# Kernel optimization log

Measured on AMD Instinct MI355X. Metric: run time of the kernel, lower is better.

The kernel has to match this reference:

```python
import jax, jax.numpy as jnp
import numpy as np

N = 100000
E = 3200000
HOP = 10

def setup_inputs() -> dict:
    key = jax.random.key(0)
    ks = jax.random.split(key, 10)
    n_in, n_hid, n_out = 512, 256, 64
    x = jax.random.normal(ks[0], (N, n_in), dtype=jnp.float32)
    edge_row = jax.random.randint(ks[1], (E,), 0, N, dtype=jnp.int32)
    edge_col = jax.random.randint(ks[2], (E,), 0, N, dtype=jnp.int32)
    # row-normalized-ish positive edge values (like a transition matrix)
    edge_vals = jax.random.uniform(ks[3], (E,), dtype=jnp.float32) / 32.0
    A2 = jax.random.uniform(ks[4], (N, 1), dtype=jnp.float32)
    # xavier-ish init scaled down for numerical sanity
    W1 = jax.random.normal(ks[5], (n_in, n_hid), dtype=jnp.float32) * (2.0 / (n_in + n_hid)) ** 0.5
    b1 = jnp.zeros((n_hid,), dtype=jnp.float32)
    W3 = jax.random.normal(ks[6], (n_hid, n_hid), dtype=jnp.float32) * (2.0 / (2 * n_hid)) ** 0.5
    b3 = jnp.zeros((n_hid,), dtype=jnp.float32)
    W2 = jax.random.normal(ks[7], (n_hid, n_out), dtype=jnp.float32) * (2.0 / (n_hid + n_out)) ** 0.5
    b2 = jnp.zeros((n_out,), dtype=jnp.float32)
    return {"x": x, "edge_row": edge_row, "edge_col": edge_col, "edge_vals": edge_vals,
            "A2": A2, "W1": W1, "b1": b1, "W3": W3, "b3": b3, "W2": W2, "b2": b2}

def _spmm(edge_row, edge_col, edge_vals, h):
    # sparse [N,N] @ dense [N,F] via gather + segment_sum
    msgs = edge_vals[:, None] * h[edge_col]          # [E, F]
    return jax.ops.segment_sum(msgs, edge_row, num_segments=N)

def reference(x, edge_row, edge_col, edge_vals, A2, W1, b1, W3, b3, W2, b2):
    # dropout layers are identity at eval time
    x0 = jax.nn.relu(x @ W1 + b1)                    # [N, n_hid]
    h = x0
    for _ in range(HOP):
        h = _spmm(edge_row, edge_col, edge_vals, h) + A2 * x0
        h = jax.nn.relu(h + h @ W3 + b3)
    return h @ W2 + b2                               # [N, n_out]
```

## Files before the change

kernel.cpp:

```cpp
#include <hip/hip_runtime.h>
#include <stdint.h>


typedef unsigned short bf16_t;
typedef __attribute__((ext_vector_type(8))) short bf16x8;
typedef __attribute__((ext_vector_type(4))) float f32x4;

__device__ __forceinline__ float bf2f(bf16_t u) {
    union { unsigned int i; float f; } v; v.i = ((unsigned int)u) << 16; return v.f;
}
__device__ __forceinline__ bf16_t f2bf(float f) {
    union { float f; unsigned int i; } v; v.f = f;
    unsigned int x = v.i;
    unsigned int r = (x + 0x7fffu + ((x >> 16) & 1u)) >> 16;
    return (bf16_t)r;
}

__global__ void zero_i32(int* __restrict__ p, int n) {
    int i = blockIdx.x * blockDim.x + threadIdx.x;
    if (i < n) p[i] = 0;
}

__global__ void transpose_w(const float* __restrict__ W, bf16_t* __restrict__ Wt,
                            int K, int N) {
    int i = blockIdx.x * blockDim.x + threadIdx.x;
    if (i < K * N) {
        int k = i / N, n = i % N;
        Wt[(size_t)n * K + k] = f2bf(W[i]);
    }
}

__global__ void count_edges(const int* __restrict__ er, int* __restrict__ cnt,
                            int E, int N) {
    int i = blockIdx.x * blockDim.x + threadIdx.x;
    if (i < E) {
        unsigned r = (unsigned)er[i];
        if (r < (unsigned)N) atomicAdd(&cnt[r], 1);
    }
}

__global__ __launch_bounds__(1024)
void scan_rows(int* cnt_cursor, int* __restrict__ row_ptr, int n) {
    __shared__ int sums[1024];
    int t = threadIdx.x;
    int chunk = (n + 1023) >> 10;
    int start = t * chunk;
    int end = min(start + chunk, n);
    int s = 0;
    for (int i = start; i < end; ++i) s += cnt_cursor[i];
    sums[t] = s;
    __syncthreads();
    for (int off = 1; off < 1024; off <<= 1) {
        int v = (t >= off) ? sums[t - off] : 0;
        __syncthreads();
        sums[t] += v;
        __syncthreads();
    }
    int run = (t == 0) ? 0 : sums[t - 1];
    for (int i = start; i < end; ++i) {
        int c = cnt_cursor[i];
        row_ptr[i] = run;
        run += c;
    }
    if (t == 1023) row_ptr[n] = sums[1023];
}

__global__ void init_bcur(const int* __restrict__ row_ptr, int* __restrict__ bcur,
                          int N, int NB) {
    int b = blockIdx.x * blockDim.x + threadIdx.x;
    if (b < NB) bcur[b] = row_ptr[min(b << 8, N)];
}

#define BIN_CHUNK 8192
#define NBMAX 392
__global__ __launch_bounds__(256)
void bin_edges(const int* __restrict__ er, const int* __restrict__ ec,
               const float* __restrict__ ev, int* __restrict__ bcur,
               int2* __restrict__ binned, int E, int N, int NB) {
    __shared__ int cnt[NBMAX];
    __shared__ int resv[NBMAX];
    int tid = threadIdx.x;
    int e0 = blockIdx.x * BIN_CHUNK;
    int n = min(BIN_CHUNK, E - e0);
    for (int b = tid; b < NB; b += 256) cnt[b] = 0;
    __syncthreads();
    for (int i = tid; i < n; i += 256) {
        unsigned r = (unsigned)er[e0 + i];
        if (r < (unsigned)N) atomicAdd(&cnt[r >> 8], 1);
    }
    __syncthreads();
    for (int b = tid; b < NB; b += 256) {
        int c = cnt[b];
        resv[b] = c ? atomicAdd(&bcur[b], c) : 0;
        cnt[b] = 0;
    }
    __syncthreads();
    for (int i = tid; i < n; i += 256) {
        unsigned r = (unsigned)er[e0 + i];
        if (r < (unsigned)N) {
            unsigned c = (unsigned)ec[e0 + i];
            float v = ev[e0 + i];
            if (c >= (unsigned)N) { c = 0; v = 0.f; }
            int b = (int)(r >> 8);
            int p = resv[b] + atomicAdd(&cnt[b], 1);
            binned[p] = make_int2((int)(((r & 255u) << 17) | c), __float_as_int(v));
        }
    }
}

#define BCAP 9216
__global__ __launch_bounds__(256)
void bucket_sort(const int* __restrict__ row_ptr, int2* __restrict__ csr, int N) {
    __shared__ int2 ent[BCAP];
    __shared__ int cnt[256];
    __shared__ int base[256];
    __shared__ int lcur[256];
    int b = blockIdx.x;
    int tid = threadIdx.x;
    int r0 = b << 8;
    int e0 = row_ptr[r0];
    int e1 = row_ptr[min(r0 + 256, N)];
    int n = e1 - e0;
    cnt[tid] = 0;
    __syncthreads();
    for (int i = tid; i < n; i += 256) {
        int2 p = csr[e0 + i];
        if (i < BCAP) ent[i] = p;
        atomicAdd(&cnt[((unsigned)p.x >> 17) & 255u], 1);
    }
    __syncthreads();
    int v0 = cnt[tid];
    for (int off = 1; off < 256; off <<= 1) {
        int u = (tid >= off) ? cnt[tid - off] : 0;
        __syncthreads();
        cnt[tid] += u;
        __syncthreads();
    }
    base[tid] = cnt[tid] - v0;
    lcur[tid] = 0;
    __syncthreads();
    for (int i = tid; i < n; i += 256) {
        int2 p = (i < BCAP) ? ent[i] : csr[e0 + i];
        int rl = (int)(((unsigned)p.x >> 17) & 255u);
        int d = base[rl] + atomicAdd(&lcur[rl], 1);
        csr[e0 + d] = make_int2(p.x & 0x1FFFF, p.y);
    }
}

__global__ __launch_bounds__(256)
void spmm_kernel(const int* __restrict__ row_ptr, const int2* __restrict__ csr,
                 const bf16_t* __restrict__ h, const bf16_t* __restrict__ x0,
                 const float* __restrict__ A2, bf16_t* __restrict__ s, int N) {
    int w = threadIdx.x >> 6;
    int lane = threadIdx.x & 63;
    int row = (blockIdx.x << 2) + w;
    if (row >= N) return;
    int fo = lane << 2;
    int base = (row << 8) + fo;
    float a2 = A2[row];
    ushort4 xv = *(const ushort4*)&x0[base];
    float acc0 = a2 * bf2f(xv.x);
    float acc1 = a2 * bf2f(xv.y);
    float acc2 = a2 * bf2f(xv.z);
    float acc3 = a2 * bf2f(xv.w);
    int e = row_ptr[row], e1 = row_ptr[row + 1];
    for (; e + 4 <= e1; e += 4) {
        int2 p0 = csr[e], p1 = csr[e + 1], p2 = csr[e + 2], p3 = csr[e + 3];
        ushort4 h0 = *(const ushort4*)&h[(p0.x << 8) + fo];
        ushort4 h1 = *(const ushort4*)&h[(p1.x << 8) + fo];
        ushort4 h2 = *(const ushort4*)&h[(p2.x << 8) + fo];
        ushort4 h3 = *(const ushort4*)&h[(p3.x << 8) + fo];
        float v0 = __int_as_float(p0.y), v1 = __int_as_float(p1.y);
        float v2 = __int_as_float(p2.y), v3 = __int_as_float(p3.y);
        acc0 += v0 * bf2f(h0.x); acc1 += v0 * bf2f(h0.y);
        acc2 += v0 * bf2f(h0.z); acc3 += v0 * bf2f(h0.w);
        acc0 += v1 * bf2f(h1.x); acc1 += v1 * bf2f(h1.y);
        acc2 += v1 * bf2f(h1.z); acc3 += v1 * bf2f(h1.w);
        acc0 += v2 * bf2f(h2.x); acc1 += v2 * bf2f(h2.y);
        acc2 += v2 * bf2f(h2.z); acc3 += v2 * bf2f(h2.w);
        acc0 += v3 * bf2f(h3.x); acc1 += v3 * bf2f(h3.y);
        acc2 += v3 * bf2f(h3.z); acc3 += v3 * bf2f(h3.w);
    }
    for (; e < e1; ++e) {
        int2 p = csr[e];
        ushort4 hv = *(const ushort4*)&h[(p.x << 8) + fo];
        float v = __int_as_float(p.y);
        acc0 += v * bf2f(hv.x); acc1 += v * bf2f(hv.y);
        acc2 += v * bf2f(hv.z); acc3 += v * bf2f(hv.w);
    }
    ushort4 o;
    o.x = f2bf(acc0); o.y = f2bf(acc1); o.z = f2bf(acc2); o.w = f2bf(acc3);
    *(ushort4*)&s[base] = o;
}

template <int WM, int WN, bool AF32, bool SKIP, bool RELU, typename CT>
__global__ __launch_bounds__(256)
void mfma_gemm(const void* __restrict__ Av, const bf16_t* __restrict__ Bt,
               const float* __restrict__ bias, CT* __restrict__ C,
               int M, int K, int Nfull) {
    constexpr int TM = WM * 64;
    constexpr int TN = WN * 64;
    __shared__ bf16_t As[TM * 32];
    __shared__ bf16_t Bs[TN * 32];
    const int tid = threadIdx.x;
    const int w = tid >> 6, lane = tid & 63;
    const int q = lane >> 4, l16 = lane & 15;
    const int bm = blockIdx.x * TM;
    const int bn = blockIdx.y * TN;
    const int wm = (w % WM) * 64;
    const int wn = (w / WM) * 64;

    f32x4 acc[4][4] = {};

    for (int k0 = 0; k0 < K; k0 += 32) {
        if constexpr (AF32) {
            const float* A = (const float*)Av;
            int row = tid >> 1;
            int gr = min(bm + row, M - 1);
            const float* src = A + (size_t)gr * K + k0 + (tid & 1) * 16;
            bf16_t* dst = As + row * 32 + (tid & 1) * 16;
            #pragma unroll
            for (int g = 0; g < 4; ++g) {
                float4 v = *(const float4*)(src + 4 * g);
                ushort4 u;
                u.x = f2bf(v.x); u.y = f2bf(v.y); u.z = f2bf(v.z); u.w = f2bf(v.w);
                *(ushort4*)(dst + 4 * g) = u;
            }
        } else {
            const bf16_t* A = (const bf16_t*)Av;
            #pragma unroll
            for (int r = 0; r < TM / 64; ++r) {
                int rowbase = r * 64 + w * 16;
                int row = rowbase + (lane >> 2);
                int gr = min(bm + row, M - 1);
                const bf16_t* gp = A + (size_t)gr * K + k0 + (lane & 3) * 8;
                bf16_t* lp = As + rowbase * 32 + lane * 8;
                __builtin_amdgcn_global_load_lds(
                    (const __attribute__((address_space(1))) unsigned int*)gp,
                    (__attribute__((address_space(3))) unsigned int*)lp, 16, 0, 0);
            }
        }
        #pragma unroll
        for (int r = 0; r < TN / 64; ++r) {
            int rowbase = r * 64 + w * 16;
            int row = rowbase + (lane >> 2);
            const bf16_t* gp = Bt + (size_t)(bn + row) * K + k0 + (lane & 3) * 8;
            bf16_t* lp = Bs + rowbase * 32 + lane * 8;
            __builtin_amdgcn_global_load_lds(
                (const __attribute__((address_space(1))) unsigned int*)gp,
                (__attribute__((address_space(3))) unsigned int*)lp, 16, 0, 0);
        }
        __syncthreads();

        bf16x8 afr[4], bfr[4];
        #pragma unroll
        for (int ms = 0; ms < 4; ++ms)
            afr[ms] = *(const bf16x8*)&As[(wm + ms * 16 + l16) * 32 + q * 8];
        #pragma unroll
        for (int ns = 0; ns < 4; ++ns)
            bfr[ns] = *(const bf16x8*)&Bs[(wn + ns * 16 + l16) * 32 + q * 8];
        #pragma unroll
        for (int ms = 0; ms < 4; ++ms)
            #pragma unroll
            for (int ns = 0; ns < 4; ++ns)
                acc[ms][ns] = __builtin_amdgcn_mfma_f32_16x16x32_bf16(
                    afr[ms], bfr[ns], acc[ms][ns], 0, 0, 0);
        __syncthreads();
    }

    const bf16_t* Askip = (const bf16_t*)Av;
    #pragma unroll
    for (int ms = 0; ms < 4; ++ms) {
        #pragma unroll
        for (int r = 0; r < 4; ++r) {
            int row = bm + wm + ms * 16 + q * 4 + r;
            if (row < M) {
                #pragma unroll
                for (int ns = 0; ns < 4; ++ns) {
                    int col = bn + wn + ns * 16 + l16;
                    float v = acc[ms][ns][r] + bias[col];
                    if constexpr (SKIP) v += bf2f(Askip[(size_t)row * K + col]);
                    if constexpr (RELU) v = fmaxf(v, 0.f);
                    if constexpr (sizeof(CT) == 2) C[(size_t)row * Nfull + col] = (CT)f2bf(v);
                    else                           C[(size_t)row * Nfull + col] = (CT)v;
                }
            }
        }
    }
}

extern "C" void kernel_launch(void* const* d_in, const int* in_sizes, int n_in,
                              void* d_out, int out_size, void* d_ws, size_t ws_size,
                              hipStream_t stream) {
    const float* x   = (const float*)d_in[0];
    const int* erow  = (const int*)d_in[1];
    const int* ecol  = (const int*)d_in[2];
    const float* ev  = (const float*)d_in[3];
    const float* A2  = (const float*)d_in[4];
    const float* W1  = (const float*)d_in[5];
    const float* b1  = (const float*)d_in[6];
    const float* W3  = (const float*)d_in[7];
    const float* b3  = (const float*)d_in[8];
    const float* W2  = (const float*)d_in[9];
    const float* b2  = (const float*)d_in[10];
    float* out = (float*)d_out;

    const int N   = in_sizes[4];
    const int E   = in_sizes[1];
    const int NIN = in_sizes[0] / N;
    const int NH  = in_sizes[6];
    const int NO  = in_sizes[10];
    if (NH != 256 || NIN != 512 || NO != 64) return;
    const int NB = (N + 255) >> 8;
    if (NB > NBMAX) return;

    char* ws = (char*)d_ws;
    size_t off = 0;
    auto alloc = [&](size_t bytes) -> void* {
        void* p = ws + off;
        off += (bytes + 255) & ~(size_t)255;
        return p;
    };
    bf16_t* x0     = (bf16_t*)alloc((size_t)N * NH * 2);
    bf16_t* hA     = (bf16_t*)alloc((size_t)N * NH * 2);
    bf16_t* hB     = (bf16_t*)alloc((size_t)N * NH * 2);
    int*   row_ptr = (int*)alloc((size_t)(N + 1) * 4);
    int*   counts  = (int*)alloc((size_t)N * 4);
    int*   bcur    = (int*)alloc((size_t)NB * 4);
    int2*  csr     = (int2*)alloc((size_t)E * 8);
    bf16_t* W1t    = (bf16_t*)alloc((size_t)NIN * NH * 2);
    bf16_t* W3t    = (bf16_t*)alloc((size_t)NH * NH * 2);
    bf16_t* W2t    = (bf16_t*)alloc((size_t)NH * NO * 2);
    if (off > ws_size) return;

    zero_i32<<<(N + 255) / 256, 256, 0, stream>>>(counts, N);
    count_edges<<<(E + 255) / 256, 256, 0, stream>>>(erow, counts, E, N);
    scan_rows<<<1, 1024, 0, stream>>>(counts, row_ptr, N);
    init_bcur<<<(NB + 255) / 256, 256, 0, stream>>>(row_ptr, bcur, N, NB);
    bin_edges<<<(E + BIN_CHUNK - 1) / BIN_CHUNK, 256, 0, stream>>>(
        erow, ecol, ev, bcur, csr, E, N, NB);
    bucket_sort<<<NB, 256, 0, stream>>>(row_ptr, csr, N);
    transpose_w<<<(NIN * NH + 255) / 256, 256, 0, stream>>>(W1, W1t, NIN, NH);
    transpose_w<<<(NH * NH + 255) / 256, 256, 0, stream>>>(W3, W3t, NH, NH);
    transpose_w<<<(NH * NO + 255) / 256, 256, 0, stream>>>(W2, W2t, NH, NO);

    dim3 g1((N + 127) / 128, NH / 128);
    mfma_gemm<2, 2, true, false, true, bf16_t><<<g1, 256, 0, stream>>>(
        x, W1t, b1, x0, N, NIN, NH);

    const bf16_t* hin = x0;
    for (int hop = 0; hop < 10; ++hop) {
        spmm_kernel<<<(N + 3) / 4, 256, 0, stream>>>(row_ptr, csr, hin, x0, A2, hB, N);
        mfma_gemm<2, 2, false, true, true, bf16_t><<<g1, 256, 0, stream>>>(
            hB, W3t, b3, hA, N, NH, NH);
        hin = hA;
    }

    dim3 g2((N + 255) / 256, 1);
    mfma_gemm<4, 1, false, false, false, float><<<g2, 256, 0, stream>>>(
        hA, W2t, b2, out, N, NH, NO);
}
```

Before: 3.439 ms.

## Split SpMM wavefront into two half-waves with 16-byte gathers and CSR prefetch

```diff
diff --git a/kernel.cpp b/kernel.cpp
--- a/kernel.cpp
+++ b/kernel.cpp
@@ -4,6 +4,7 @@
 
 typedef unsigned short bf16_t;
 typedef __attribute__((ext_vector_type(8))) short bf16x8;
+typedef __attribute__((ext_vector_type(8))) unsigned short u16x8;
 typedef __attribute__((ext_vector_type(4))) float f32x4;
 
 __device__ __forceinline__ float bf2f(bf16_t u) {
@@ -147,6 +148,12 @@
     }
 }
 
+__device__ __forceinline__ void fma8(float* acc, float v, u16x8 hv) {
+    #pragma unroll
+    for (int k = 0; k < 8; ++k)
+        acc[k] = fmaf(v, bf2f((bf16_t)hv[k]), acc[k]);
+}
+
 __global__ __launch_bounds__(256)
 void spmm_kernel(const int* __restrict__ row_ptr, const int2* __restrict__ csr,
                  const bf16_t* __restrict__ h, const bf16_t* __restrict__ x0,
@@ -155,42 +162,64 @@
     int lane = threadIdx.x & 63;
     int row = (blockIdx.x << 2) + w;
     if (row >= N) return;
-    int fo = lane << 2;
+    int half = lane >> 5;
+    int l32 = lane & 31;
+    int fo = l32 << 3;
     int base = (row << 8) + fo;
-    float a2 = A2[row];
-    ushort4 xv = *(const ushort4*)&x0[base];
-    float acc0 = a2 * bf2f(xv.x);
-    float acc1 = a2 * bf2f(xv.y);
-    float acc2 = a2 * bf2f(xv.z);
-    float acc3 = a2 * bf2f(xv.w);
+
+    float acc[8];
+    if (half == 0) {
+        float a2 = A2[row];
+        u16x8 xv = *(const u16x8*)&x0[base];
+        #pragma unroll
+        for (int k = 0; k < 8; ++k) acc[k] = a2 * bf2f((bf16_t)xv[k]);
+    } else {
+        #pragma unroll
+        for (int k = 0; k < 8; ++k) acc[k] = 0.f;
+    }
+
     int e = row_ptr[row], e1 = row_ptr[row + 1];
-    for (; e + 4 <= e1; e += 4) {
-        int2 p0 = csr[e], p1 = csr[e + 1], p2 = csr[e + 2], p3 = csr[e + 3];
-        ushort4 h0 = *(const ushort4*)&h[(p0.x << 8) + fo];
-        ushort4 h1 = *(const ushort4*)&h[(p1.x << 8) + fo];
-        ushort4 h2 = *(const ushort4*)&h[(p2.x << 8) + fo];
-        ushort4 h3 = *(const ushort4*)&h[(p3.x << 8) + fo];
-        float v0 = __int_as_float(p0.y), v1 = __int_as_float(p1.y);
-        float v2 = __int_as_float(p2.y), v3 = __int_as_float(p3.y);
-        acc0 += v0 * bf2f(h0.x); acc1 += v0 * bf2f(h0.y);
-        acc2 += v0 * bf2f(h0.z); acc3 += v0 * bf2f(h0.w);
-        acc0 += v1 * bf2f(h1.x); acc1 += v1 * bf2f(h1.y);
-        acc2 += v1 * bf2f(h1.z); acc3 += v1 * bf2f(h1.w);
-        acc0 += v2 * bf2f(h2.x); acc1 += v2 * bf2f(h2.y);
-        acc2 += v2 * bf2f(h2.z); acc3 += v2 * bf2f(h2.w);
-        acc0 += v3 * bf2f(h3.x); acc1 += v3 * bf2f(h3.y);
-        acc2 += v3 * bf2f(h3.z); acc3 += v3 * bf2f(h3.w);
-    }
-    for (; e < e1; ++e) {
+    int nb = (e1 - e) >> 3;
+    int2 q0, q1, q2, q3;
+    if (nb > 0) {
+        int eb = e + half;
+        q0 = csr[eb]; q1 = csr[eb + 2]; q2 = csr[eb + 4]; q3 = csr[eb + 6];
+    }
+    for (int b = 0; b < nb; ++b) {
+        int2 p0 = q0, p1 = q1, p2 = q2, p3 = q3;
+        if (b + 1 < nb) {
+            int eb = e + 8 + half;
+            q0 = csr[eb]; q1 = csr[eb + 2]; q2 = csr[eb + 4]; q3 = csr[eb + 6];
+        }
+        u16x8 h0 = *(const u16x8*)&h[(p0.x << 8) + fo];
+        u16x8 h1 = *(const u16x8*)&h[(p1.x << 8) + fo];
+        u16x8 h2 = *(const u16x8*)&h[(p2.x << 8) + fo];
+        u16x8 h3 = *(const u16x8*)&h[(p3.x << 8) + fo];
+        fma8(acc, __int_as_float(p0.y), h0);
+        fma8(acc, __int_as_float(p1.y), h1);
+        fma8(acc, __int_as_float(p2.y), h2);
+        fma8(acc, __int_as_float(p3.y), h3);
+        e += 8;
+    }
+    for (; e + 2 <= e1; e += 2) {
+        int2 p = csr[e + half];
+        u16x8 hv = *(const u16x8*)&h[(p.x << 8) + fo];
+        fma8(acc, __int_as_float(p.y), hv);
+    }
+    if (e < e1 && half == 0) {
         int2 p = csr[e];
-        ushort4 hv = *(const ushort4*)&h[(p.x << 8) + fo];
-        float v = __int_as_float(p.y);
-        acc0 += v * bf2f(hv.x); acc1 += v * bf2f(hv.y);
-        acc2 += v * bf2f(hv.z); acc3 += v * bf2f(hv.w);
-    }
-    ushort4 o;
-    o.x = f2bf(acc0); o.y = f2bf(acc1); o.z = f2bf(acc2); o.w = f2bf(acc3);
-    *(ushort4*)&s[base] = o;
+        u16x8 hv = *(const u16x8*)&h[(p.x << 8) + fo];
+        fma8(acc, __int_as_float(p.y), hv);
+    }
+
+    #pragma unroll
+    for (int k = 0; k < 8; ++k) acc[k] += __shfl_xor(acc[k], 32, 64);
+    if (half == 0) {
+        u16x8 o;
+        #pragma unroll
+        for (int k = 0; k < 8; ++k) o[k] = f2bf(acc[k]);
+        *(u16x8*)&s[base] = o;
+    }
 }
 
 template <int WM, int WN, bool AF32, bool SKIP, bool RELU, typename CT>
```

After: 3.457 ms. No clear change (+0.5%).
